# Optimization experiments

Measured on AMD Instinct MI355X. Metric: run time of the kernel, lower is better.

Reference implementation:

```python
import jax, jax.numpy as jnp
import numpy as np

N, T, E = 20000, 4, 320000
IN_F, H_F, OUT_F, HEADS = 32, 16, 16, 8
NEG_SLOPE = 0.2


def gat_layer(x, W, al, ar, b, src, dst, n_nodes, heads, f_out):
    # x: [N, T, Fin], W: [Fin, heads*f_out], al/ar: [heads, f_out], b: [heads*f_out]
    feat = (x @ W).reshape(x.shape[0], x.shape[1], heads, f_out)      # [N,T,H,F]
    el = (feat * al).sum(-1)                                          # [N,T,H]
    er = (feat * ar).sum(-1)                                          # [N,T,H]
    e = jax.nn.leaky_relu(el[src] + er[dst], NEG_SLOPE)               # [E,T,H]
    # segment softmax over incoming edges of each destination node
    m = jax.lax.stop_gradient(jax.ops.segment_max(e, dst, num_segments=n_nodes))
    ex = jnp.exp(e - m[dst])
    s = jax.ops.segment_sum(ex, dst, num_segments=n_nodes)
    alpha = ex / s[dst]                                               # [E,T,H]
    msg = feat[src] * alpha[..., None]                                # [E,T,H,F]
    out = jax.ops.segment_sum(msg, dst, num_segments=n_nodes)
    return out + b.reshape(1, 1, heads, f_out)


def setup_inputs() -> dict:
    key = jax.random.key(0)
    ks = jax.random.split(key, 12)
    x = jax.random.normal(ks[0], (N, T, IN_F), dtype=jnp.float32)
    src = jax.random.randint(ks[1], (E,), 0, N)
    dst = jax.random.randint(ks[2], (E,), 0, N)
    s = 0.1
    W1 = jax.random.normal(ks[3], (IN_F, HEADS * H_F), dtype=jnp.float32) * s
    al1 = jax.random.normal(ks[4], (HEADS, H_F), dtype=jnp.float32) * s
    ar1 = jax.random.normal(ks[5], (HEADS, H_F), dtype=jnp.float32) * s
    b1 = jnp.zeros((HEADS * H_F,), dtype=jnp.float32)
    W2 = jax.random.normal(ks[6], (HEADS * H_F, OUT_F), dtype=jnp.float32) * s
    al2 = jax.random.normal(ks[7], (1, OUT_F), dtype=jnp.float32) * s
    ar2 = jax.random.normal(ks[8], (1, OUT_F), dtype=jnp.float32) * s
    b2 = jnp.zeros((OUT_F,), dtype=jnp.float32)
    return {"x": x, "src": src, "dst": dst, "W1": W1, "al1": al1, "ar1": ar1,
            "b1": b1, "W2": W2, "al2": al2, "ar2": ar2, "b2": b2}


def reference(x, src, dst, W1, al1, ar1, b1, W2, al2, ar2, b2):
    n = x.shape[0]
    h = gat_layer(x, W1, al1, ar1, b1, src, dst, n, HEADS, H_F)   # [N,T,H,F]
    h = h.reshape(n, h.shape[1], -1)                              # [N,T,H*F]
    h = gat_layer(h, W2, al2, ar2, b2, src, dst, n, 1, OUT_F)     # [N,T,1,OUT]
    return h.squeeze(2)                                           # [N,T,OUT]
```

## Files before the change

kernel.cpp:

```cpp
#include <hip/hip_runtime.h>
#include <hip/hip_fp16.h>
#include <math.h>

#define NN 20000
#define TT 4
#define EE 320000
#define NT (NN*TT)
#define H1 8
#define C1 128
#define IN_F 32
#define OUT_F 16
#define CAP 96
#define SCAT_BLOCKS 313
#define XCAST_BLOCKS 1250

typedef _Float16 h8 __attribute__((ext_vector_type(8)));
typedef float f32x4 __attribute__((ext_vector_type(4)));

__device__ __forceinline__ float lrelu_exp(float e) {
  e = (e >= 0.f) ? e : 0.2f * e;
  return __expf(e);
}

__global__ __launch_bounds__(256) void k_front(
    const float* __restrict__ x, const float* __restrict__ W1,
    const float* __restrict__ al1, const float* __restrict__ ar1,
    const float* __restrict__ W2, const float* __restrict__ al2,
    const float* __restrict__ ar2,
    const int4* __restrict__ src4, const int4* __restrict__ dst4,
    int* __restrict__ cnt, int* __restrict__ csr96,
    __half* __restrict__ xh, float* __restrict__ el1, float* __restrict__ er1,
    __half* __restrict__ W1hp, __half* __restrict__ W2pp) {
  __shared__ h8 ELERs[64];
  int b = blockIdx.x;
  int tid = threadIdx.x;
  if (b < SCAT_BLOCKS) {
    int e4 = b * 256 + tid;
    if (e4 < EE / 4) {
      int4 s = src4[e4];
      int4 d = dst4[e4];
      int p0 = atomicAdd(&cnt[d.x], 1); csr96[d.x * CAP + p0] = s.x;
      int p1 = atomicAdd(&cnt[d.y], 1); csr96[d.y * CAP + p1] = s.y;
      int p2 = atomicAdd(&cnt[d.z], 1); csr96[d.z * CAP + p2] = s.z;
      int p3 = atomicAdd(&cnt[d.w], 1); csr96[d.w * CAP + p3] = s.w;
    }
    return;
  }
  if (b == SCAT_BLOCKS) {
    for (int idx = tid; idx < 8 * 512; idx += 256) {
      int tile = idx >> 9;
      int rem = idx & 511;
      int lane = rem >> 3, j = rem & 7;
      int k = (lane >> 4) * 8 + j;
      int n = lane & 15;
      W1hp[idx] = __float2half(W1[k * C1 + tile * 16 + n]);
    }
    for (int idx = tid; idx < 8 * 512; idx += 256) {
      int tile = idx >> 9;
      int rem = idx & 511;
      int lane = rem >> 3, j = rem & 7;
      int ks = tile & 3;
      int k = ks * 32 + (lane >> 4) * 8 + j;
      int n = lane & 15;
      float v = 0.f;
      if (tile < 4) {
        v = W2[k * OUT_F + n];
      } else if (n == 0) {
        float s = 0.f;
        for (int f = 0; f < 16; ++f) s += W2[k * OUT_F + f] * al2[f];
        v = s;
      } else if (n == 1) {
        float s = 0.f;
        for (int f = 0; f < 16; ++f) s += W2[k * OUT_F + f] * ar2[f];
        v = s;
      }
      W2pp[idx] = __float2half(v);
    }
    return;
  }
  {
    __half* E = (__half*)ELERs;
    for (int idx = tid; idx < 512; idx += 256) {
      int lane = idx >> 3, j = idx & 7;
      int k = (lane >> 4) * 8 + j;
      int n = lane & 15;
      int hh_ = n & 7;
      const float* a = (n < 8) ? al1 : ar1;
      float s = 0.f;
      for (int f = 0; f < 16; ++f) s += W1[k * C1 + hh_ * 16 + f] * a[hh_ * 16 + f];
      E[idx] = __float2half(s);
    }
  }
  __syncthreads();
  int wave = tid >> 6, lane = tid & 63;
  int m = lane & 15, quad = lane >> 4;
  int rowbase = (b - SCAT_BLOCKS - 1) * 64 + wave * 16;
  int row = rowbase + m;
  const float4* xp = (const float4*)(x + row * IN_F + quad * 8);
  float4 a0 = xp[0], a1 = xp[1];
  h8 af;
  af[0] = (_Float16)a0.x; af[1] = (_Float16)a0.y;
  af[2] = (_Float16)a0.z; af[3] = (_Float16)a0.w;
  af[4] = (_Float16)a1.x; af[5] = (_Float16)a1.y;
  af[6] = (_Float16)a1.z; af[7] = (_Float16)a1.w;
  *(h8*)(xh + (size_t)row * IN_F + quad * 8) = af;
  {
    h8 bf = ELERs[lane];
    f32x4 c = {0.f, 0.f, 0.f, 0.f};
    c = __builtin_amdgcn_mfma_f32_16x16x32_f16(af, bf, c, 0, 0, 0);
#pragma unroll
    for (int r = 0; r < 4; ++r) {
      int orow = rowbase + quad * 4 + r;
      if (m < 8) el1[orow * H1 + m] = c[r];
      else       er1[orow * H1 + (m - 8)] = c[r];
    }
  }
}

__global__ __launch_bounds__(256) void k_agg1x(
    const __half* __restrict__ xh,
    const float* __restrict__ el1,
    const float* __restrict__ er1,
    const int* __restrict__ cnt, const int* __restrict__ csr96,
    __half* __restrict__ aggx) {
  int tid = threadIdx.x;
  int wv = tid >> 6, lane = tid & 63;
  int n = blockIdx.x * 4 + wv;
  int slot = lane >> 1;
  int t = lane >> 4;
  int hf = lane & 1;
  float er_i = er1[(size_t)n * 32 + slot];
  int deg = cnt[n];
  const int* eb = csr96 + (size_t)n * CAP;
  float acc[16];
#pragma unroll
  for (int k = 0; k < 16; ++k) acc[k] = 0.f;
  float l = 0.f;
  for (int chunk = 0; chunk < deg; chunk += 64) {
    int m = min(64, deg - chunk);
    int sv = (lane < m) ? eb[chunk + lane] : 0;
    int iters = (m + 3) >> 2;
    for (int g = 0; g < iters; ++g) {
      int j = g * 4;
      int s0 = __builtin_amdgcn_readlane(sv, j + 0);
      int s1 = __builtin_amdgcn_readlane(sv, j + 1);
      int s2 = __builtin_amdgcn_readlane(sv, j + 2);
      int s3 = __builtin_amdgcn_readlane(sv, j + 3);
      float ew0 = el1[(size_t)s0 * 32 + slot];
      float ew1 = el1[(size_t)s1 * 32 + slot];
      float ew2 = el1[(size_t)s2 * 32 + slot];
      float ew3 = el1[(size_t)s3 * 32 + slot];
      const __half* x0 = xh + (size_t)(s0 * 4 + t) * 32 + hf * 16;
      const __half* x1 = xh + (size_t)(s1 * 4 + t) * 32 + hf * 16;
      const __half* x2 = xh + (size_t)(s2 * 4 + t) * 32 + hf * 16;
      const __half* x3 = xh + (size_t)(s3 * 4 + t) * 32 + hf * 16;
      h8 a0 = *(const h8*)x0, b0 = *(const h8*)(x0 + 8);
      h8 a1 = *(const h8*)x1, b1_ = *(const h8*)(x1 + 8);
      h8 a2 = *(const h8*)x2, b2_ = *(const h8*)(x2 + 8);
      h8 a3 = *(const h8*)x3, b3_ = *(const h8*)(x3 + 8);
#define CONSUME(K, EW, XA, XB)                                    \
      {                                                           \
        float w_ = lrelu_exp(EW + er_i);                          \
        w_ = (j + K < m) ? w_ : 0.f;                              \
        l += w_;                                                  \
        _Pragma("unroll")                                         \
        for (int q = 0; q < 8; ++q) {                             \
          acc[q]     = fmaf(w_, (float)XA[q], acc[q]);            \
          acc[8 + q] = fmaf(w_, (float)XB[q], acc[8 + q]);        \
        }                                                         \
      }
      CONSUME(0, ew0, a0, b0) CONSUME(1, ew1, a1, b1_)
      CONSUME(2, ew2, a2, b2_) CONSUME(3, ew3, a3, b3_)
#undef CONSUME
    }
  }
  float inv = (l > 0.f) ? (1.f / l) : 0.f;
  h8 r0, r1;
#pragma unroll
  for (int q = 0; q < 8; ++q) {
    r0[q] = (_Float16)(acc[q] * inv);
    r1[q] = (_Float16)(acc[8 + q] * inv);
  }
  int hh_ = slot & 7;
  __half* op = aggx + (size_t)(n * 4 + t) * 256 + hh_ * 32 + hf * 16;
  *(h8*)op = r0;
  *(h8*)(op + 8) = r1;
}

__global__ __launch_bounds__(256) void k_mid2(
    const __half* __restrict__ aggx,
    const __half* __restrict__ W1hp, const float* __restrict__ b1,
    const __half* __restrict__ W2pp,
    __half* __restrict__ feat2h, float* __restrict__ el2, float* __restrict__ er2) {
  __shared__ __half hs[4][16][C1];
  int tid = threadIdx.x;
  int wave = tid >> 6, lane = tid & 63;
  int m = lane & 15, quad = lane >> 4;
  int rowbase = blockIdx.x * 64 + wave * 16;
  const h8* bp1 = (const h8*)W1hp;
#pragma unroll
  for (int hh_ = 0; hh_ < 8; ++hh_) {
    h8 af = *(const h8*)(aggx + (size_t)(rowbase + m) * 256 + hh_ * 32 + quad * 8);
    f32x4 c = {0.f, 0.f, 0.f, 0.f};
    c = __builtin_amdgcn_mfma_f32_16x16x32_f16(af, bp1[hh_ * 64 + lane], c, 0, 0, 0);
    float bv = b1[hh_ * 16 + m];
#pragma unroll
    for (int r = 0; r < 4; ++r)
      hs[wave][quad * 4 + r][hh_ * 16 + m] = __float2half(c[r] + bv);
  }
  const h8* bp2 = (const h8*)W2pp;
  f32x4 cF = {0.f, 0.f, 0.f, 0.f};
  f32x4 cE = {0.f, 0.f, 0.f, 0.f};
#pragma unroll
  for (int ks = 0; ks < 4; ++ks) {
    h8 af = *(const h8*)&hs[wave][m][ks * 32 + quad * 8];
    cF = __builtin_amdgcn_mfma_f32_16x16x32_f16(af, bp2[ks * 64 + lane], cF, 0, 0, 0);
    cE = __builtin_amdgcn_mfma_f32_16x16x32_f16(af, bp2[(4 + ks) * 64 + lane], cE, 0, 0, 0);
  }
#pragma unroll
  for (int r = 0; r < 4; ++r) {
    int orow = rowbase + quad * 4 + r;
    feat2h[(size_t)orow * OUT_F + m] = __float2half(cF[r]);
    if (m == 0) el2[orow] = cE[r];
    if (m == 1) er2[orow] = cE[r];
  }
}

__global__ __launch_bounds__(256) void k_agg2x(
    const __half* __restrict__ feat2h,
    const float* __restrict__ el2, const float* __restrict__ er2,
    const int* __restrict__ cnt, const int* __restrict__ csr96,
    const float* __restrict__ b2, float* __restrict__ out) {
  int tid = threadIdx.x;
  int wv = tid >> 6, lane = tid & 63;
  int n = blockIdx.x * 4 + wv;
  int t = lane >> 4, f = lane & 15;
  float ern = er2[n * 4 + t];
  int deg = cnt[n];
  const int* eb = csr96 + (size_t)n * CAP;
  float acc = 0.f, l = 0.f;
  for (int chunk = 0; chunk < deg; chunk += 64) {
    int m = min(64, deg - chunk);
    int sv = (lane < m) ? eb[chunk + lane] : 0;
    int iters = (m + 7) >> 3;
    for (int g = 0; g < iters; ++g) {
      int j = g * 8;
      int s0 = __builtin_amdgcn_readlane(sv, j + 0);
      int s1 = __builtin_amdgcn_readlane(sv, j + 1);
      int s2 = __builtin_amdgcn_readlane(sv, j + 2);
      int s3 = __builtin_amdgcn_readlane(sv, j + 3);
      int s4 = __builtin_amdgcn_readlane(sv, j + 4);
      int s5 = __builtin_amdgcn_readlane(sv, j + 5);
      int s6 = __builtin_amdgcn_readlane(sv, j + 6);
      int s7 = __builtin_amdgcn_readlane(sv, j + 7);
      float e0 = el2[s0 * 4 + t];
      float e1 = el2[s1 * 4 + t];
      float e2 = el2[s2 * 4 + t];
      float e3 = el2[s3 * 4 + t];
      float e4 = el2[s4 * 4 + t];
      float e5 = el2[s5 * 4 + t];
      float e6 = el2[s6 * 4 + t];
      float e7 = el2[s7 * 4 + t];
      __half f0 = feat2h[(size_t)(s0 * 4 + t) * OUT_F + f];
      __half f1 = feat2h[(size_t)(s1 * 4 + t) * OUT_F + f];
      __half f2 = feat2h[(size_t)(s2 * 4 + t) * OUT_F + f];
      __half f3 = feat2h[(size_t)(s3 * 4 + t) * OUT_F + f];
      __half f4 = feat2h[(size_t)(s4 * 4 + t) * OUT_F + f];
      __half f5 = feat2h[(size_t)(s5 * 4 + t) * OUT_F + f];
      __half f6 = feat2h[(size_t)(s6 * 4 + t) * OUT_F + f];
      __half f7 = feat2h[(size_t)(s7 * 4 + t) * OUT_F + f];
#define CONSUME(K, EW, FV)                                        \
      {                                                           \
        float w_ = lrelu_exp(EW + ern);                           \
        w_ = (j + K < m) ? w_ : 0.f;                              \
        l += w_;                                                  \
        acc = fmaf(w_, __half2float(FV), acc);                    \
      }
      CONSUME(0, e0, f0) CONSUME(1, e1, f1)
      CONSUME(2, e2, f2) CONSUME(3, e3, f3)
      CONSUME(4, e4, f4) CONSUME(5, e5, f5)
      CONSUME(6, e6, f6) CONSUME(7, e7, f7)
#undef CONSUME
    }
  }
  float inv = (l > 0.f) ? (1.f / l) : 0.f;
  out[(size_t)(n * 4 + t) * OUT_F + f] = acc * inv + b2[f];
}

extern "C" void kernel_launch(void* const* d_in, const int* in_sizes, int n_in,
                              void* d_out, int out_size, void* d_ws, size_t ws_size,
                              hipStream_t stream) {
  const float* x   = (const float*)d_in[0];
  const int*   src = (const int*)d_in[1];
  const int*   dst = (const int*)d_in[2];
  const float* W1  = (const float*)d_in[3];
  const float* al1 = (const float*)d_in[4];
  const float* ar1 = (const float*)d_in[5];
  const float* b1  = (const float*)d_in[6];
  const float* W2  = (const float*)d_in[7];
  const float* al2 = (const float*)d_in[8];
  const float* ar2 = (const float*)d_in[9];
  const float* b2  = (const float*)d_in[10];
  float* out = (float*)d_out;

  char* w = (char*)d_ws;
  __half* xh     = (__half*)w; w += (size_t)NT * IN_F * 2;
  __half* aggx   = (__half*)w; w += (size_t)NT * 256 * 2;
  __half* feat2h = (__half*)w; w += (size_t)NT * OUT_F * 2;
  float*  el1    = (float*)w;  w += (size_t)NT * H1 * 4;
  float*  er1    = (float*)w;  w += (size_t)NT * H1 * 4;
  float*  el2    = (float*)w;  w += (size_t)NT * 4;
  float*  er2    = (float*)w;  w += (size_t)NT * 4;
  __half* W1hp   = (__half*)w; w += (size_t)8 * 512 * 2;
  __half* W2pp   = (__half*)w; w += (size_t)8 * 512 * 2;
  int* cnt     = (int*)w;      w += (size_t)NN * 4;
  int* csr96   = (int*)w;      w += (size_t)NN * CAP * 4;

  hipMemsetAsync(cnt, 0, NN * sizeof(int), stream);

  k_front<<<SCAT_BLOCKS + 1 + XCAST_BLOCKS, 256, 0, stream>>>(
      x, W1, al1, ar1, W2, al2, ar2, (const int4*)src, (const int4*)dst,
      cnt, csr96, xh, el1, er1, W1hp, W2pp);
  k_agg1x<<<NN / 4, 256, 0, stream>>>(xh, el1, er1, cnt, csr96, aggx);
  k_mid2<<<NT / 64, 256, 0, stream>>>(aggx, W1hp, b1, W2pp, feat2h, el2, er2);
  k_agg2x<<<NN / 4, 256, 0, stream>>>(feat2h, el2, er2, cnt, csr96, b2, out);
}
```

Measured before the change: 164.5 us.

## Stage neighbor features through LDS with cooperative coalesced loads in agg1x

In the layer-1 aggregation kernel, each wave now fetches the full 128-half feature rows and 32-float logit rows for 8 neighbors at once with coalesced per-lane vector loads into shared memory. It then consumes them from LDS, instead of each lane gathering its own slice of 4 neighbors directly from global memory. The goal is fewer, wider global transactions and more edges in flight per iteration. In exchange it adds LDS traffic and relies on intra-wave ordering without explicit barriers. Out-of-range lanes fetch row sv=0 (node 0), which is masked by the weight.

```diff
diff --git a/kernel.cpp b/kernel.cpp
--- a/kernel.cpp
+++ b/kernel.cpp
@@ -123,12 +123,16 @@
     const float* __restrict__ er1,
     const int* __restrict__ cnt, const int* __restrict__ csr96,
     __half* __restrict__ aggx) {
+  __shared__ __half xs[4][8][128];
+  __shared__ float  es[4][8][32];
   int tid = threadIdx.x;
   int wv = tid >> 6, lane = tid & 63;
   int n = blockIdx.x * 4 + wv;
   int slot = lane >> 1;
   int t = lane >> 4;
   int hf = lane & 1;
+  int ej = lane >> 3;
+  int eo = lane & 7;
   float er_i = er1[(size_t)n * 32 + slot];
   int deg = cnt[n];
   const int* eb = csr96 + (size_t)n * CAP;
@@ -139,39 +143,30 @@
   for (int chunk = 0; chunk < deg; chunk += 64) {
     int m = min(64, deg - chunk);
     int sv = (lane < m) ? eb[chunk + lane] : 0;
-    int iters = (m + 3) >> 2;
+    int iters = (m + 7) >> 3;
     for (int g = 0; g < iters; ++g) {
-      int j = g * 4;
-      int s0 = __builtin_amdgcn_readlane(sv, j + 0);
-      int s1 = __builtin_amdgcn_readlane(sv, j + 1);
-      int s2 = __builtin_amdgcn_readlane(sv, j + 2);
-      int s3 = __builtin_amdgcn_readlane(sv, j + 3);
-      float ew0 = el1[(size_t)s0 * 32 + slot];
-      float ew1 = el1[(size_t)s1 * 32 + slot];
-      float ew2 = el1[(size_t)s2 * 32 + slot];
-      float ew3 = el1[(size_t)s3 * 32 + slot];
-      const __half* x0 = xh + (size_t)(s0 * 4 + t) * 32 + hf * 16;
-      const __half* x1 = xh + (size_t)(s1 * 4 + t) * 32 + hf * 16;
-      const __half* x2 = xh + (size_t)(s2 * 4 + t) * 32 + hf * 16;
-      const __half* x3 = xh + (size_t)(s3 * 4 + t) * 32 + hf * 16;
-      h8 a0 = *(const h8*)x0, b0 = *(const h8*)(x0 + 8);
-      h8 a1 = *(const h8*)x1, b1_ = *(const h8*)(x1 + 8);
-      h8 a2 = *(const h8*)x2, b2_ = *(const h8*)(x2 + 8);
-      h8 a3 = *(const h8*)x3, b3_ = *(const h8*)(x3 + 8);
-#define CONSUME(K, EW, XA, XB)                                    \
-      {                                                           \
-        float w_ = lrelu_exp(EW + er_i);                          \
-        w_ = (j + K < m) ? w_ : 0.f;                              \
-        l += w_;                                                  \
-        _Pragma("unroll")                                         \
-        for (int q = 0; q < 8; ++q) {                             \
-          acc[q]     = fmaf(w_, (float)XA[q], acc[q]);            \
-          acc[8 + q] = fmaf(w_, (float)XB[q], acc[8 + q]);        \
-        }                                                         \
+      int j = g * 8;
+      int sj = __shfl(sv, j + ej);
+      const h8* xp = (const h8*)(xh + (size_t)sj * 128 + eo * 16);
+      h8 xa = xp[0], xb = xp[1];
+      float4 ev = *(const float4*)(el1 + (size_t)sj * 32 + eo * 4);
+      *(h8*)&xs[wv][ej][eo * 16]     = xa;
+      *(h8*)&xs[wv][ej][eo * 16 + 8] = xb;
+      *(float4*)&es[wv][ej][eo * 4]  = ev;
+#pragma unroll
+      for (int k = 0; k < 8; ++k) {
+        float ew = es[wv][k][slot];
+        float w_ = lrelu_exp(ew + er_i);
+        w_ = (j + k < m) ? w_ : 0.f;
+        l += w_;
+        h8 fa = *(const h8*)&xs[wv][k][t * 32 + hf * 16];
+        h8 fb = *(const h8*)&xs[wv][k][t * 32 + hf * 16 + 8];
+#pragma unroll
+        for (int q = 0; q < 8; ++q) {
+          acc[q]     = fmaf(w_, (float)fa[q], acc[q]);
+          acc[8 + q] = fmaf(w_, (float)fb[q], acc[8 + q]);
+        }
       }
-      CONSUME(0, ew0, a0, b0) CONSUME(1, ew1, a1, b1_)
-      CONSUME(2, ew2, a2, b2_) CONSUME(3, ew3, a3, b3_)
-#undef CONSUME
     }
   }
   float inv = (l > 0.f) ? (1.f / l) : 0.f;
```

Result: no change. 166.5 us (+1.2%).
